# Performance work log

Hardware: AMD Instinct MI355X
Metric: run time of the kernel (lower is better)

Reference implementation:

```python
import jax, jax.numpy as jnp
import numpy as np

D_MODEL = 1024
NUM_HEADS = 16


def setup_inputs() -> dict:
    key = jax.random.key(0)
    ks = jax.random.split(key, 5)
    B, T, d = 2, 2048, D_MODEL
    s = 1.0 / np.sqrt(d)
    return {
        "x": jax.random.normal(ks[0], (B, T, d), dtype=jnp.float32),
        "W_kqv": jax.random.normal(ks[1], (d, 3 * d), dtype=jnp.float32) * s,
        "b_kqv": jax.random.normal(ks[2], (3 * d,), dtype=jnp.float32) * 0.02,
        "W_o": jax.random.normal(ks[3], (d, d), dtype=jnp.float32) * s,
        "b_o": jax.random.normal(ks[4], (d,), dtype=jnp.float32) * 0.02,
    }


def reference(x, W_kqv, b_kqv, W_o, b_o):
    B, T, d = x.shape
    H = NUM_HEADS
    dk = d // H
    kqv = x @ W_kqv + b_kqv                      # [B, T, 3d]
    # source splits as contiguous chunks in order K, Q, V
    K, Q, V = jnp.split(kqv, 3, axis=-1)
    # [B, T, d] -> [B, H, T, dk]
    to_heads = lambda t: t.reshape(B, T, H, dk).transpose(0, 2, 1, 3)
    K, Q, V = to_heads(K), to_heads(Q), to_heads(V)
    scores = jnp.einsum("bhtd,bhsd->bhts", Q, K)  # [B, H, T, T]
    causal = jnp.triu(jnp.ones((T, T), dtype=bool), k=1)
    scores = jnp.where(causal, -jnp.inf, scores)
    attn = jax.nn.softmax(scores / jnp.sqrt(jnp.asarray(dk, x.dtype)), axis=-1)
    out = jnp.einsum("bhts,bhsd->bhtd", attn, V)  # [B, H, T, dk]
    out = out.transpose(0, 2, 1, 3).reshape(B, T, d)
    return out @ W_o + b_o
```

## Files before the change

kernel.cpp:

```cpp
#include <hip/hip_runtime.h>
#include <hip/hip_bf16.h>
#include <stdint.h>
#include <math.h>

using bf16x8 = __attribute__((ext_vector_type(8))) short;
using f32x4  = __attribute__((ext_vector_type(4))) float;

#define NHEAD  16
#define DK     64
#define TSEQ   2048
#define DMODEL 1024
#define MTOT   4096

static __device__ __forceinline__ ushort f2bf(float f) {
  union { float f; uint32_t u; } v; v.f = f;
  return (ushort)((v.u + 0x7FFFu + ((v.u >> 16) & 1u)) >> 16);
}

static __device__ __forceinline__ void gload_lds16(const ushort* g, ushort* l) {
  typedef __attribute__((address_space(1))) const uint32_t gu32;
  typedef __attribute__((address_space(3))) uint32_t lu32;
  __builtin_amdgcn_global_load_lds((gu32*)g, (lu32*)l, 16, 0, 0);
}

__global__ void cvt_bf16_kernel(const float* __restrict__ in, ushort* __restrict__ out, int n) {
  int i = (blockIdx.x * 256 + threadIdx.x) * 8;
  const int stride = gridDim.x * 256 * 8;
  for (; i < n; i += stride) {
    const float4* p = (const float4*)(in + i);
    float4 a = p[0], b = p[1];
    bf16x8 v;
    v[0]=(short)f2bf(a.x); v[1]=(short)f2bf(a.y); v[2]=(short)f2bf(a.z); v[3]=(short)f2bf(a.w);
    v[4]=(short)f2bf(b.x); v[5]=(short)f2bf(b.y); v[6]=(short)f2bf(b.z); v[7]=(short)f2bf(b.w);
    *(bf16x8*)(out + i) = v;
  }
}

__global__ __launch_bounds__(256) void transpose_cvt_kernel(const float* __restrict__ W,
                                                            ushort* __restrict__ Wt, int K, int N) {
  __shared__ ushort tl[64][66];
  const int n0 = blockIdx.x * 64, k0 = blockIdx.y * 64;
  const int c = threadIdx.x & 63, r0 = threadIdx.x >> 6;
#pragma unroll
  for (int i = 0; i < 64; i += 4)
    tl[i + r0][c] = f2bf(W[(size_t)(k0 + i + r0) * N + n0 + c]);
  __syncthreads();
#pragma unroll
  for (int i = 0; i < 64; i += 4)
    Wt[(size_t)(n0 + i + r0) * K + k0 + c] = tl[c][i + r0];
}

__global__ __launch_bounds__(256) void transpose_v_kernel(const ushort* __restrict__ V,
                                                          ushort* __restrict__ Vt) {
  __shared__ ushort tl[64][66];
  const int bh = blockIdx.y, t0 = blockIdx.x * 64;
  const int c = threadIdx.x & 63, r0 = threadIdx.x >> 6;
  const ushort* Vb = V + (size_t)bh * TSEQ * DK;
  ushort* Vtb = Vt + (size_t)bh * DK * TSEQ;
#pragma unroll
  for (int i = 0; i < 64; i += 4)
    tl[i + r0][c] = Vb[(size_t)(t0 + i + r0) * DK + c];
  __syncthreads();
#pragma unroll
  for (int i = 0; i < 64; i += 4)
    Vtb[(size_t)(i + r0) * TSEQ + t0 + c] = tl[c][i + r0];
}

template <int MODE>
__global__ __launch_bounds__(256, 2)
void gemm_bt_kernel(const ushort* __restrict__ A, const ushort* __restrict__ Bt,
                    const float* __restrict__ bias,
                    ushort* __restrict__ oK, ushort* __restrict__ oQ, ushort* __restrict__ oV,
                    float* __restrict__ oF, int N, int K) {
  __shared__ ushort As[128 * 32];
  __shared__ ushort Bs[128 * 32];
  const int tid = threadIdx.x;
  const int w = tid >> 6, lane = tid & 63;
  const int m0 = blockIdx.y * 128, n0 = blockIdx.x * 128;
  const int wr = (w >> 1) * 64, wc = (w & 1) * 64;

  const int e0 = ((w * 2 + 0) * 64 + lane) * 8;
  const int e1 = ((w * 2 + 1) * 64 + lane) * 8;
  const ushort* pA0 = A  + (size_t)(m0 + (e0 >> 5)) * K + (e0 & 31);
  const ushort* pA1 = A  + (size_t)(m0 + (e1 >> 5)) * K + (e1 & 31);
  const ushort* pB0 = Bt + (size_t)(n0 + (e0 >> 5)) * K + (e0 & 31);
  const ushort* pB1 = Bt + (size_t)(n0 + (e1 >> 5)) * K + (e1 & 31);

  f32x4 acc[4][4];
#pragma unroll
  for (int i = 0; i < 4; i++)
#pragma unroll
    for (int j = 0; j < 4; j++) acc[i][j] = (f32x4){0.f, 0.f, 0.f, 0.f};

  const int aro = (wr + (lane & 15)) * 32 + (lane >> 4) * 8;
  const int bro = (wc + (lane & 15)) * 32 + (lane >> 4) * 8;

  for (int k0 = 0; k0 < K; k0 += 32) {
    __syncthreads();
    gload_lds16(pA0 + k0, &As[e0]);
    gload_lds16(pA1 + k0, &As[e1]);
    gload_lds16(pB0 + k0, &Bs[e0]);
    gload_lds16(pB1 + k0, &Bs[e1]);
    __syncthreads();
    bf16x8 af[4], bfr[4];
#pragma unroll
    for (int i = 0; i < 4; i++) af[i]  = *(const bf16x8*)&As[aro + i * 16 * 32];
#pragma unroll
    for (int j = 0; j < 4; j++) bfr[j] = *(const bf16x8*)&Bs[bro + j * 16 * 32];
#pragma unroll
    for (int i = 0; i < 4; i++)
#pragma unroll
      for (int j = 0; j < 4; j++)
        acc[i][j] = __builtin_amdgcn_mfma_f32_16x16x32_bf16(af[i], bfr[j], acc[i][j], 0, 0, 0);
  }

  const int rbase = m0 + wr + (lane >> 4) * 4;
  const int cbase = n0 + wc + (lane & 15);
#pragma unroll
  for (int i = 0; i < 4; i++) {
#pragma unroll
    for (int j = 0; j < 4; j++) {
      const int gn = cbase + j * 16;
      const float bv = bias[gn];
#pragma unroll
      for (int jj = 0; jj < 4; jj++) {
        const int gm = rbase + i * 16 + jj;
        const float val = acc[i][j][jj] + bv;
        if (MODE == 0) {
          const int sel = gn >> 10, cc = gn & 1023;
          const int h = cc >> 6, dd = cc & 63;
          const int bb = gm >> 11, t = gm & 2047;
          ushort* dst = (sel == 0) ? oK : (sel == 1) ? oQ : oV;
          dst[((size_t)((bb * NHEAD + h) * TSEQ + t)) * DK + dd] = f2bf(val);
        } else {
          oF[(size_t)gm * N + gn] = val;
        }
      }
    }
  }
}

__global__ __launch_bounds__(256, 4)
void attn_kernel(const ushort* __restrict__ Qb, const ushort* __restrict__ Kb,
                 const ushort* __restrict__ Vtb, ushort* __restrict__ O) {
  __shared__ ushort Ks[2][64 * 64];
  __shared__ ushort Vs[2][64 * 64];
  __shared__ ushort Ps[4][16 * 64];

  const int bid = blockIdx.x;
  const int xcd = bid & 7, jj_ = bid >> 3;
  const int bh = xcd + 8 * (jj_ >> 5);
  const int qi = 31 - (jj_ & 31);
  const int q0 = qi * 64;
  const int bb = bh >> 4, h = bh & 15;
  const int tid = threadIdx.x, w = tid >> 6, lane = tid & 63;
  const int l15 = lane & 15, l4 = lane >> 4;

  const ushort* Qp = Qb + ((size_t)bh * TSEQ + q0 + w * 16) * DK;
  bf16x8 qf[2];
#pragma unroll
  for (int c = 0; c < 2; c++)
    qf[c] = *(const bf16x8*)(Qp + l15 * DK + c * 32 + l4 * 8);

  f32x4 oacc[4];
  float mrun[4], lrun[4];
#pragma unroll
  for (int n = 0; n < 4; n++) oacc[n] = (f32x4){0.f, 0.f, 0.f, 0.f};
#pragma unroll
  for (int r = 0; r < 4; r++) { mrun[r] = -INFINITY; lrun[r] = 0.f; }

  const int Bl0 = w * 128 + lane, Bl1 = Bl0 + 64;
  const int sr0 = Bl0 >> 3, sc0 = ((Bl0 & 7) ^ (sr0 & 7)) * 8;
  const int sr1 = Bl1 >> 3, sc1 = ((Bl1 & 7) ^ (sr1 & 7)) * 8;
  const ushort* Kp0 = Kb  + (size_t)bh * TSEQ * DK + sr0 * DK + sc0;
  const ushort* Kp1 = Kb  + (size_t)bh * TSEQ * DK + sr1 * DK + sc1;
  const ushort* Vp0 = Vtb + (size_t)bh * DK * TSEQ + sr0 * TSEQ + sc0;
  const ushort* Vp1 = Vtb + (size_t)bh * DK * TSEQ + sr1 * TSEQ + sc1;

  ushort* Pw = &Ps[w][0];
  const int nt = qi + 1;

  gload_lds16(Kp0, &Ks[0][Bl0 * 8]);
  gload_lds16(Kp1, &Ks[0][Bl1 * 8]);
  gload_lds16(Vp0, &Vs[0][Bl0 * 8]);
  gload_lds16(Vp1, &Vs[0][Bl1 * 8]);
  asm volatile("s_waitcnt vmcnt(0)" ::: "memory");
  __builtin_amdgcn_s_barrier();

  for (int ti = 0; ti < nt; ti++) {
    const int s0 = ti * 64, cur = ti & 1;

    if (ti + 1 < nt) {
      const int sn = (ti + 1) * 64, nb = cur ^ 1;
      gload_lds16(Kp0 + sn * DK, &Ks[nb][Bl0 * 8]);
      gload_lds16(Kp1 + sn * DK, &Ks[nb][Bl1 * 8]);
      gload_lds16(Vp0 + sn, &Vs[nb][Bl0 * 8]);
      gload_lds16(Vp1 + sn, &Vs[nb][Bl1 * 8]);
    }

    f32x4 s[4];
    __builtin_amdgcn_s_setprio(1);
#pragma unroll
    for (int n = 0; n < 4; n++) {
      const int krow = n * 16 + l15;
      const int sw = (krow & 7) << 4;
      bf16x8 kf0 = *(const bf16x8*)((const char*)&Ks[cur][0] + krow * 128 + ((l4 * 16) ^ sw));
      bf16x8 kf1 = *(const bf16x8*)((const char*)&Ks[cur][0] + krow * 128 + ((64 + l4 * 16) ^ sw));
      f32x4 z = (f32x4){0.f, 0.f, 0.f, 0.f};
      z = __builtin_amdgcn_mfma_f32_16x16x32_bf16(qf[0], kf0, z, 0, 0, 0);
      z = __builtin_amdgcn_mfma_f32_16x16x32_bf16(qf[1], kf1, z, 0, 0, 0);
      s[n] = z;
    }
    __builtin_amdgcn_s_setprio(0);

    const bool need_mask = (s0 >= q0);
#pragma unroll
    for (int r = 0; r < 4; r++) {
      const int row = q0 + w * 16 + l4 * 4 + r;
      float v0 = s[0][r] * 0.125f, v1 = s[1][r] * 0.125f;
      float v2 = s[2][r] * 0.125f, v3 = s[3][r] * 0.125f;
      if (need_mask) {
        if (s0 +  0 + l15 > row) v0 = -INFINITY;
        if (s0 + 16 + l15 > row) v1 = -INFINITY;
        if (s0 + 32 + l15 > row) v2 = -INFINITY;
        if (s0 + 48 + l15 > row) v3 = -INFINITY;
      }
      float tm = fmaxf(fmaxf(v0, v1), fmaxf(v2, v3));
      tm = fmaxf(tm, __shfl_xor(tm, 1));
      tm = fmaxf(tm, __shfl_xor(tm, 2));
      tm = fmaxf(tm, __shfl_xor(tm, 4));
      tm = fmaxf(tm, __shfl_xor(tm, 8));
      const float nm  = fmaxf(mrun[r], tm);
      const float scl = __expf(mrun[r] - nm);
      mrun[r] = nm;
      v0 = __expf(v0 - nm); v1 = __expf(v1 - nm);
      v2 = __expf(v2 - nm); v3 = __expf(v3 - nm);
      float rs = v0 + v1 + v2 + v3;
      rs += __shfl_xor(rs, 1); rs += __shfl_xor(rs, 2);
      rs += __shfl_xor(rs, 4); rs += __shfl_xor(rs, 8);
      lrun[r] = lrun[r] * scl + rs;
      s[0][r] = v0; s[1][r] = v1; s[2][r] = v2; s[3][r] = v3;
      oacc[0][r] *= scl; oacc[1][r] *= scl;
      oacc[2][r] *= scl; oacc[3][r] *= scl;
    }

#pragma unroll
    for (int r = 0; r < 4; r++) {
      const int prow = l4 * 4 + r;
      const int sw = (prow & 7) << 4;
      char* rp = (char*)Pw + prow * 128;
#pragma unroll
      for (int n = 0; n < 4; n++) {
        const int cb = (n * 16 + l15) * 2;
        *(ushort*)(rp + (cb ^ sw)) = f2bf(s[n][r]);
      }
    }

    bf16x8 vf[4][2];
#pragma unroll
    for (int n = 0; n < 4; n++) {
      const int vrow = n * 16 + l15;
      const int sw = (vrow & 7) << 4;
      vf[n][0] = *(const bf16x8*)((const char*)&Vs[cur][0] + vrow * 128 + ((l4 * 16) ^ sw));
      vf[n][1] = *(const bf16x8*)((const char*)&Vs[cur][0] + vrow * 128 + ((64 + l4 * 16) ^ sw));
    }
    {
      const int prow = l15;
      const int sw = (prow & 7) << 4;
      bf16x8 pf0 = *(const bf16x8*)((const char*)Pw + prow * 128 + ((l4 * 16) ^ sw));
      bf16x8 pf1 = *(const bf16x8*)((const char*)Pw + prow * 128 + ((64 + l4 * 16) ^ sw));
      __builtin_amdgcn_s_setprio(1);
#pragma unroll
      for (int n = 0; n < 4; n++) {
        oacc[n] = __builtin_amdgcn_mfma_f32_16x16x32_bf16(pf0, vf[n][0], oacc[n], 0, 0, 0);
        oacc[n] = __builtin_amdgcn_mfma_f32_16x16x32_bf16(pf1, vf[n][1], oacc[n], 0, 0, 0);
      }
      __builtin_amdgcn_s_setprio(0);
    }

    asm volatile("s_waitcnt vmcnt(0)" ::: "memory");
    __builtin_amdgcn_s_barrier();
  }

#pragma unroll
  for (int r = 0; r < 4; r++) {
    const float inv = 1.f / lrun[r];
    const int t = q0 + w * 16 + l4 * 4 + r;
    ushort* orow = O + ((size_t)bb * TSEQ + t) * DMODEL + h * DK;
#pragma unroll
    for (int n = 0; n < 4; n++)
      orow[n * 16 + l15] = f2bf(oacc[n][r] * inv);
  }
}

extern "C" void kernel_launch(void* const* d_in, const int* in_sizes, int n_in,
                              void* d_out, int out_size, void* d_ws, size_t ws_size,
                              hipStream_t stream) {
  (void)in_sizes; (void)n_in; (void)out_size; (void)ws_size;
  const float* x    = (const float*)d_in[0];
  const float* Wkqv = (const float*)d_in[1];
  const float* bkqv = (const float*)d_in[2];
  const float* Wo   = (const float*)d_in[3];
  const float* bo   = (const float*)d_in[4];
  float* out = (float*)d_out;

  char* ws = (char*)d_ws;
  const size_t MB = 1024 * 1024;
  ushort* x_bf   = (ushort*)(ws + 0);
  ushort* wkqv_t = (ushort*)(ws + 8 * MB);
  ushort* wo_t   = (ushort*)(ws + 14 * MB);
  ushort* Kbuf   = (ushort*)(ws + 16 * MB);
  ushort* Qbuf   = (ushort*)(ws + 24 * MB);
  ushort* Vbuf   = (ushort*)(ws + 32 * MB);
  ushort* Vtbuf  = (ushort*)(ws + 40 * MB);
  ushort* AObuf  = (ushort*)(ws + 48 * MB);

  cvt_bf16_kernel<<<2048, 256, 0, stream>>>(x, x_bf, MTOT * DMODEL);
  transpose_cvt_kernel<<<dim3(3072 / 64, 1024 / 64), 256, 0, stream>>>(Wkqv, wkqv_t, 1024, 3072);
  transpose_cvt_kernel<<<dim3(1024 / 64, 1024 / 64), 256, 0, stream>>>(Wo, wo_t, 1024, 1024);
  gemm_bt_kernel<0><<<dim3(3072 / 128, 4096 / 128), 256, 0, stream>>>(
      x_bf, wkqv_t, bkqv, Kbuf, Qbuf, Vbuf, nullptr, 3072, 1024);
  transpose_v_kernel<<<dim3(TSEQ / 64, 32), 256, 0, stream>>>(Vbuf, Vtbuf);
  attn_kernel<<<1024, 256, 0, stream>>>(Qbuf, Kbuf, Vtbuf, AObuf);
  gemm_bt_kernel<1><<<dim3(1024 / 128, 4096 / 128), 256, 0, stream>>>(
      AObuf, wo_t, bo, nullptr, nullptr, nullptr, out, 1024, 1024);
}
```

Measured before the change: 255.9 us.

## Rework attention with 32x32 MFMA, register-resident P and 128-row query tiles

```diff
diff --git a/kernel.cpp b/kernel.cpp
--- a/kernel.cpp
+++ b/kernel.cpp
@@ -5,6 +5,7 @@
 
 using bf16x8 = __attribute__((ext_vector_type(8))) short;
 using f32x4  = __attribute__((ext_vector_type(4))) float;
+using f32x16 = __attribute__((ext_vector_type(16))) float;
 
 #define NHEAD  16
 #define DK     64
@@ -12,9 +13,17 @@
 #define DMODEL 1024
 #define MTOT   4096
 
+#define QSCALE 0.18033688011112042f
+
 static __device__ __forceinline__ ushort f2bf(float f) {
   union { float f; uint32_t u; } v; v.f = f;
   return (ushort)((v.u + 0x7FFFu + ((v.u >> 16) & 1u)) >> 16);
+}
+
+static __device__ __forceinline__ uint32_t cvtpk_bf16(float lo, float hi) {
+  uint32_t r;
+  asm("v_cvt_pk_bf16_f32 %0, %1, %2" : "=v"(r) : "v"(lo), "v"(hi));
+  return r;
 }
 
 static __device__ __forceinline__ void gload_lds16(const ushort* g, ushort* l) {
@@ -125,13 +134,14 @@
 #pragma unroll
       for (int jj = 0; jj < 4; jj++) {
         const int gm = rbase + i * 16 + jj;
-        const float val = acc[i][j][jj] + bv;
+        float val = acc[i][j][jj] + bv;
         if (MODE == 0) {
           const int sel = gn >> 10, cc = gn & 1023;
-          const int h = cc >> 6, dd = cc & 63;
-          const int bb = gm >> 11, t = gm & 2047;
+          const int hh = cc >> 6, dd = cc & 63;
+          const int bbx = gm >> 11, t = gm & 2047;
+          if (sel == 1) val *= QSCALE;
           ushort* dst = (sel == 0) ? oK : (sel == 1) ? oQ : oV;
-          dst[((size_t)((bb * NHEAD + h) * TSEQ + t)) * DK + dd] = f2bf(val);
+          dst[((size_t)((bbx * NHEAD + hh) * TSEQ + t)) * DK + dd] = f2bf(val);
         } else {
           oF[(size_t)gm * N + gn] = val;
         }
@@ -140,34 +150,32 @@
   }
 }
 
-__global__ __launch_bounds__(256, 4)
+__global__ __launch_bounds__(256, 2)
 void attn_kernel(const ushort* __restrict__ Qb, const ushort* __restrict__ Kb,
                  const ushort* __restrict__ Vtb, ushort* __restrict__ O) {
   __shared__ ushort Ks[2][64 * 64];
   __shared__ ushort Vs[2][64 * 64];
-  __shared__ ushort Ps[4][16 * 64];
 
   const int bid = blockIdx.x;
-  const int xcd = bid & 7, jj_ = bid >> 3;
-  const int bh = xcd + 8 * (jj_ >> 5);
-  const int qi = 31 - (jj_ & 31);
-  const int q0 = qi * 64;
-  const int bb = bh >> 4, h = bh & 15;
+  const int xcd = bid & 7, j = bid >> 3;
+  const int bh = xcd + 8 * (j >> 4);
+  const int qi = 15 - (j & 15);
+  const int q0 = qi * 128;
+  const int bb = bh >> 4, hd = bh & 15;
   const int tid = threadIdx.x, w = tid >> 6, lane = tid & 63;
-  const int l15 = lane & 15, l4 = lane >> 4;
-
-  const ushort* Qp = Qb + ((size_t)bh * TSEQ + q0 + w * 16) * DK;
-  bf16x8 qf[2];
-#pragma unroll
-  for (int c = 0; c < 2; c++)
-    qf[c] = *(const bf16x8*)(Qp + l15 * DK + c * 32 + l4 * 8);
-
-  f32x4 oacc[4];
-  float mrun[4], lrun[4];
-#pragma unroll
-  for (int n = 0; n < 4; n++) oacc[n] = (f32x4){0.f, 0.f, 0.f, 0.f};
-#pragma unroll
-  for (int r = 0; r < 4; r++) { mrun[r] = -INFINITY; lrun[r] = 0.f; }
+  const int l31 = lane & 31, h = lane >> 5;
+  const int qrow = q0 + w * 32 + l31;
+
+  const ushort* Qp = Qb + ((size_t)bh * TSEQ + qrow) * DK;
+  bf16x8 qf[4];
+#pragma unroll
+  for (int c = 0; c < 4; c++)
+    qf[c] = *(const bf16x8*)(Qp + c * 16 + h * 8);
+
+  f32x16 oacc0, oacc1;
+#pragma unroll
+  for (int r = 0; r < 16; r++) { oacc0[r] = 0.f; oacc1[r] = 0.f; }
+  float mrun = -INFINITY, lrun = 0.f;
 
   const int Bl0 = w * 128 + lane, Bl1 = Bl0 + 64;
   const int sr0 = Bl0 >> 3, sc0 = ((Bl0 & 7) ^ (sr0 & 7)) * 8;
@@ -177,8 +185,7 @@
   const ushort* Vp0 = Vtb + (size_t)bh * DK * TSEQ + sr0 * TSEQ + sc0;
   const ushort* Vp1 = Vtb + (size_t)bh * DK * TSEQ + sr1 * TSEQ + sc1;
 
-  ushort* Pw = &Ps[w][0];
-  const int nt = qi + 1;
+  const int nt = 2 * qi + 2;
 
   gload_lds16(Kp0, &Ks[0][Bl0 * 8]);
   gload_lds16(Kp1, &Ks[0][Bl1 * 8]);
@@ -198,98 +205,108 @@
       gload_lds16(Vp1 + sn, &Vs[nb][Bl1 * 8]);
     }
 
-    f32x4 s[4];
-    __builtin_amdgcn_s_setprio(1);
-#pragma unroll
-    for (int n = 0; n < 4; n++) {
-      const int krow = n * 16 + l15;
-      const int sw = (krow & 7) << 4;
-      bf16x8 kf0 = *(const bf16x8*)((const char*)&Ks[cur][0] + krow * 128 + ((l4 * 16) ^ sw));
-      bf16x8 kf1 = *(const bf16x8*)((const char*)&Ks[cur][0] + krow * 128 + ((64 + l4 * 16) ^ sw));
-      f32x4 z = (f32x4){0.f, 0.f, 0.f, 0.f};
-      z = __builtin_amdgcn_mfma_f32_16x16x32_bf16(qf[0], kf0, z, 0, 0, 0);
-      z = __builtin_amdgcn_mfma_f32_16x16x32_bf16(qf[1], kf1, z, 0, 0, 0);
-      s[n] = z;
-    }
-    __builtin_amdgcn_s_setprio(0);
-
-    const bool need_mask = (s0 >= q0);
-#pragma unroll
-    for (int r = 0; r < 4; r++) {
-      const int row = q0 + w * 16 + l4 * 4 + r;
-      float v0 = s[0][r] * 0.125f, v1 = s[1][r] * 0.125f;
-      float v2 = s[2][r] * 0.125f, v3 = s[3][r] * 0.125f;
-      if (need_mask) {
-        if (s0 +  0 + l15 > row) v0 = -INFINITY;
-        if (s0 + 16 + l15 > row) v1 = -INFINITY;
-        if (s0 + 32 + l15 > row) v2 = -INFINITY;
-        if (s0 + 48 + l15 > row) v3 = -INFINITY;
-      }
-      float tm = fmaxf(fmaxf(v0, v1), fmaxf(v2, v3));
-      tm = fmaxf(tm, __shfl_xor(tm, 1));
-      tm = fmaxf(tm, __shfl_xor(tm, 2));
-      tm = fmaxf(tm, __shfl_xor(tm, 4));
-      tm = fmaxf(tm, __shfl_xor(tm, 8));
-      const float nm  = fmaxf(mrun[r], tm);
-      const float scl = __expf(mrun[r] - nm);
-      mrun[r] = nm;
-      v0 = __expf(v0 - nm); v1 = __expf(v1 - nm);
-      v2 = __expf(v2 - nm); v3 = __expf(v3 - nm);
-      float rs = v0 + v1 + v2 + v3;
-      rs += __shfl_xor(rs, 1); rs += __shfl_xor(rs, 2);
-      rs += __shfl_xor(rs, 4); rs += __shfl_xor(rs, 8);
-      lrun[r] = lrun[r] * scl + rs;
-      s[0][r] = v0; s[1][r] = v1; s[2][r] = v2; s[3][r] = v3;
-      oacc[0][r] *= scl; oacc[1][r] *= scl;
-      oacc[2][r] *= scl; oacc[3][r] *= scl;
-    }
-
-#pragma unroll
-    for (int r = 0; r < 4; r++) {
-      const int prow = l4 * 4 + r;
-      const int sw = (prow & 7) << 4;
-      char* rp = (char*)Pw + prow * 128;
-#pragma unroll
-      for (int n = 0; n < 4; n++) {
-        const int cb = (n * 16 + l15) * 2;
-        *(ushort*)(rp + (cb ^ sw)) = f2bf(s[n][r]);
-      }
-    }
-
-    bf16x8 vf[4][2];
-#pragma unroll
-    for (int n = 0; n < 4; n++) {
-      const int vrow = n * 16 + l15;
-      const int sw = (vrow & 7) << 4;
-      vf[n][0] = *(const bf16x8*)((const char*)&Vs[cur][0] + vrow * 128 + ((l4 * 16) ^ sw));
-      vf[n][1] = *(const bf16x8*)((const char*)&Vs[cur][0] + vrow * 128 + ((64 + l4 * 16) ^ sw));
-    }
-    {
-      const int prow = l15;
-      const int sw = (prow & 7) << 4;
-      bf16x8 pf0 = *(const bf16x8*)((const char*)Pw + prow * 128 + ((l4 * 16) ^ sw));
-      bf16x8 pf1 = *(const bf16x8*)((const char*)Pw + prow * 128 + ((64 + l4 * 16) ^ sw));
+    const bool active = (s0 <= q0 + w * 32 + 31);
+    if (active) {
+      f32x16 ps0, ps1;
+#pragma unroll
+      for (int r = 0; r < 16; r++) { ps0[r] = 0.f; ps1[r] = 0.f; }
+      const char* Kbase = (const char*)&Ks[cur][0];
       __builtin_amdgcn_s_setprio(1);
 #pragma unroll
-      for (int n = 0; n < 4; n++) {
-        oacc[n] = __builtin_amdgcn_mfma_f32_16x16x32_bf16(pf0, vf[n][0], oacc[n], 0, 0, 0);
-        oacc[n] = __builtin_amdgcn_mfma_f32_16x16x32_bf16(pf1, vf[n][1], oacc[n], 0, 0, 0);
+      for (int c = 0; c < 4; c++) {
+        const int r0 = l31, r1 = 32 + l31;
+        bf16x8 kf0 = *(const bf16x8*)(Kbase + r0 * 128 + ((c * 32 + h * 16) ^ ((r0 & 7) << 4)));
+        bf16x8 kf1 = *(const bf16x8*)(Kbase + r1 * 128 + ((c * 32 + h * 16) ^ ((r1 & 7) << 4)));
+        ps0 = __builtin_amdgcn_mfma_f32_32x32x16_bf16(kf0, qf[c], ps0, 0, 0, 0);
+        ps1 = __builtin_amdgcn_mfma_f32_32x32x16_bf16(kf1, qf[c], ps1, 0, 0, 0);
       }
       __builtin_amdgcn_s_setprio(0);
+
+      if (s0 + 63 > q0 + w * 32) {
+#pragma unroll
+        for (int r = 0; r < 16; r++) {
+          const int kv0 = s0 + (r & 3) + 8 * (r >> 2) + 4 * h;
+          if (kv0 > qrow)      ps0[r] = -INFINITY;
+          if (kv0 + 32 > qrow) ps1[r] = -INFINITY;
+        }
+      }
+
+      float pm = ps0[0];
+#pragma unroll
+      for (int r = 1; r < 16; r++) pm = fmaxf(pm, ps0[r]);
+#pragma unroll
+      for (int r = 0; r < 16; r++) pm = fmaxf(pm, ps1[r]);
+      pm = fmaxf(pm, __shfl_xor(pm, 32));
+
+      if (!__all(pm <= mrun + 8.0f)) {
+        const float nm = fmaxf(mrun, pm);
+        const float scl = exp2f(mrun - nm);
+        lrun *= scl;
+#pragma unroll
+        for (int r = 0; r < 16; r++) { oacc0[r] *= scl; oacc1[r] *= scl; }
+        mrun = nm;
+      }
+
+#pragma unroll
+      for (int r = 0; r < 16; r++) ps0[r] = exp2f(ps0[r] - mrun);
+#pragma unroll
+      for (int r = 0; r < 16; r++) ps1[r] = exp2f(ps1[r] - mrun);
+      float rs = 0.f;
+#pragma unroll
+      for (int r = 0; r < 16; r++) rs += ps0[r] + ps1[r];
+      rs += __shfl_xor(rs, 32);
+      lrun += rs;
+
+      uint32_t w0[2][4], w1[2][4];
+#pragma unroll
+      for (int a = 0; a < 4; a++) {
+        w0[0][a] = cvtpk_bf16(ps0[4 * a + 0], ps0[4 * a + 1]);
+        w1[0][a] = cvtpk_bf16(ps0[4 * a + 2], ps0[4 * a + 3]);
+        w0[1][a] = cvtpk_bf16(ps1[4 * a + 0], ps1[4 * a + 1]);
+        w1[1][a] = cvtpk_bf16(ps1[4 * a + 2], ps1[4 * a + 3]);
+      }
+
+      const char* Vbase = (const char*)&Vs[cur][0];
+#pragma unroll
+      for (int s = 0; s < 2; s++) {
+#pragma unroll
+        for (int u = 0; u < 2; u++) {
+          const int t = 2 * s + u;
+          const uint32_t sw0 = h ? w0[s][2 * u] : w0[s][2 * u + 1];
+          const uint32_t sw1 = h ? w1[s][2 * u] : w1[s][2 * u + 1];
+          const uint32_t rx0 = (uint32_t)__shfl_xor((int)sw0, 32);
+          const uint32_t rx1 = (uint32_t)__shfl_xor((int)sw1, 32);
+          int4 pw;
+          pw.x = h ? (int)rx0 : (int)w0[s][2 * u];
+          pw.y = h ? (int)rx1 : (int)w1[s][2 * u];
+          pw.z = h ? (int)w0[s][2 * u + 1] : (int)rx0;
+          pw.w = h ? (int)w1[s][2 * u + 1] : (int)rx1;
+          const bf16x8 pf = __builtin_bit_cast(bf16x8, pw);
+
+          const int vr0 = l31, vr1 = 32 + l31;
+          bf16x8 vf0 = *(const bf16x8*)(Vbase + vr0 * 128 + ((t * 32 + h * 16) ^ ((vr0 & 7) << 4)));
+          bf16x8 vf1 = *(const bf16x8*)(Vbase + vr1 * 128 + ((t * 32 + h * 16) ^ ((vr1 & 7) << 4)));
+          __builtin_amdgcn_s_setprio(1);
+          oacc0 = __builtin_amdgcn_mfma_f32_32x32x16_bf16(vf0, pf, oacc0, 0, 0, 0);
+          oacc1 = __builtin_amdgcn_mfma_f32_32x32x16_bf16(vf1, pf, oacc1, 0, 0, 0);
+          __builtin_amdgcn_s_setprio(0);
+        }
+      }
     }
 
     asm volatile("s_waitcnt vmcnt(0)" ::: "memory");
     __builtin_amdgcn_s_barrier();
   }
 
-#pragma unroll
-  for (int r = 0; r < 4; r++) {
-    const float inv = 1.f / lrun[r];
-    const int t = q0 + w * 16 + l4 * 4 + r;
-    ushort* orow = O + ((size_t)bb * TSEQ + t) * DMODEL + h * DK;
-#pragma unroll
-    for (int n = 0; n < 4; n++)
-      orow[n * 16 + l15] = f2bf(oacc[n][r] * inv);
+  const float inv = 1.f / lrun;
+  ushort* orow = O + ((size_t)bb * TSEQ + qrow) * DMODEL + hd * DK;
+#pragma unroll
+  for (int r = 0; r < 16; r += 2) {
+    const int d0 = (r & 3) + 8 * (r >> 2) + 4 * h;
+    const uint32_t v0 = (uint32_t)f2bf(oacc0[r] * inv) | ((uint32_t)f2bf(oacc0[r + 1] * inv) << 16);
+    const uint32_t v1 = (uint32_t)f2bf(oacc1[r] * inv) | ((uint32_t)f2bf(oacc1[r + 1] * inv) << 16);
+    *(uint32_t*)(orow + d0)      = v0;
+    *(uint32_t*)(orow + 32 + d0) = v1;
   }
 }
 
@@ -321,7 +338,7 @@
   gemm_bt_kernel<0><<<dim3(3072 / 128, 4096 / 128), 256, 0, stream>>>(
       x_bf, wkqv_t, bkqv, Kbuf, Qbuf, Vbuf, nullptr, 3072, 1024);
   transpose_v_kernel<<<dim3(TSEQ / 64, 32), 256, 0, stream>>>(Vbuf, Vtbuf);
-  attn_kernel<<<1024, 256, 0, stream>>>(Qbuf, Kbuf, Vtbuf, AObuf);
+  attn_kernel<<<512, 256, 0, stream>>>(Qbuf, Kbuf, Vtbuf, AObuf);
   gemm_bt_kernel<1><<<dim3(1024 / 128, 4096 / 128), 256, 0, stream>>>(
       AObuf, wo_t, bo, nullptr, nullptr, nullptr, out, 1024, 1024);
 }
```

After: 217.9 us. -14.8%, faster.
